# Optimization experiments

Measured on AMD Instinct MI355X. Metric: run time of the kernel, lower is better.

Reference implementation:

```python
import jax, jax.numpy as jnp
import numpy as np

K_POW = 3.0
EPS = 1e-6

def _weight1(d, r):
    # (1 - (d/r)^2)^k for d < r else 0; guard base before float power
    base = jnp.where(d < r, 1.0 - (d / r) ** 2, 0.0)
    return base ** K_POW

def _weight2(d, r):
    # 1 for d < r/2; (1 - ((2d-r)/r)^2)^k for r/2 <= d < r; else 0
    band = (d >= r / 2) & (d < r)
    base = jnp.where(band, 1.0 - ((2.0 * d - r) / r) ** 2, 0.0)
    return jnp.where(d < r / 2, 1.0, base ** K_POW)

def setup_inputs() -> dict:
    key = jax.random.key(0)
    ks = jax.random.split(key, 10)
    n, p, L = 4096, 128, 32
    x = jax.random.uniform(ks[0], (n, p), dtype=jnp.float32)
    s = 0.05
    return {
        "x": x,
        "r0": jnp.float32(4.0),
        "r1": jnp.float32(2.0),
        "r2": jnp.float32(4.0),
        "We1": jax.random.normal(ks[1], (L, p), jnp.float32) * s,
        "be1": jnp.zeros((L,), jnp.float32),
        "We2": jax.random.normal(ks[2], (L, L), jnp.float32) * s,
        "be2": jnp.zeros((L,), jnp.float32),
        "Wd1": jax.random.normal(ks[3], (L, L), jnp.float32) * s,
        "bd1": jnp.zeros((L,), jnp.float32),
        "Wd2": jax.random.normal(ks[4], (p, L), jnp.float32) * s,
        "bd2": jnp.zeros((p,), jnp.float32),
    }

def _mr_layer(x, r0, r1, r2):
    y = x  # y = x.clone()
    x2 = jnp.sum(x * x, axis=-1)
    d2 = x2[:, None] + x2[None, :] - 2.0 * (x @ x.T)  # (n, n)
    dist = jnp.sqrt(jnp.maximum(d2, 1e-12))
    md = dist.max()
    # torch reassigns r to max_dist when r > max_dist -> min(r, max_dist)
    r0e = jnp.minimum(r0, md)
    r1e = jnp.minimum(r1, md)
    r2e = jnp.minimum(r2, md)
    # inds = any(dist <= r0) is all-true (diag is ~0), so no row selection needed
    alpha = _weight1(dist, r0e)
    alpha = alpha / jnp.sum(alpha, axis=0, keepdims=True)
    mu = alpha.T @ x  # (n, p)
    mu = jnp.where(jnp.isnan(mu), y, mu)
    U = y - mu  # (n, p); contraction direction per point
    # projection scalar ps[i,j] = <x_i - y_j, U_j>, avoiding (n,n,p) diff tensor
    ps = x @ U.T - jnp.sum(y * U, axis=-1)[None, :]  # (n, n)
    u_norm2 = jnp.sum(U * U, axis=-1)[None, :]  # (1, n)
    dist_u2 = jnp.maximum(ps ** 2 * u_norm2, EPS)
    dist_v = jnp.sqrt(jnp.maximum(dist ** 2 - dist_u2, EPS))
    dist_u = jnp.sqrt(dist_u2)
    beta = _weight2(dist_v, r1e) * _weight2(dist_u, r2e)
    beta = beta / jnp.sum(beta, axis=0, keepdims=True)
    e_Z = beta.T @ x
    e_Z = jnp.where(jnp.isnan(e_Z), y, e_Z)
    return e_Z

def reference(x, r0, r1, r2, We1, be1, We2, be2, Wd1, bd1, Wd2, bd2):
    y = _mr_layer(x, r0, r1, r2)
    # encoder: Linear -> GELU(exact) -> Linear
    h = jax.nn.gelu(y @ We1.T + be1, approximate=False)
    z = h @ We2.T + be2
    # decoder: Linear -> GELU(exact) -> Linear -> Sigmoid
    h2 = jax.nn.gelu(z @ Wd1.T + bd1, approximate=False)
    x_hat = jax.nn.sigmoid(h2 @ Wd2.T + bd2)
    # loss = lam_recon * MSE(x, x_hat); lam_topo = lam_geom = 0
    return jnp.mean((x - x_hat) ** 2)
```

## Files before the change

kernel.cpp:

```cpp
#include <hip/hip_runtime.h>
#include <math.h>

#define N 4096
#define P 128
#define LDIM 32
#define CHUNKS 8
#define ITILES 4

typedef unsigned int u32;
typedef unsigned short u16;
typedef short s16x8 __attribute__((ext_vector_type(8)));
typedef float f32x4 __attribute__((ext_vector_type(4)));

__device__ __forceinline__ u16 f2b(float f) {
  u32 u = __float_as_uint(f);
  u += 0x7fffu + ((u >> 16) & 1u);
  return (u16)(u >> 16);
}
__device__ __forceinline__ float b2f(u16 h) { return __uint_as_float(((u32)h) << 16); }

__device__ __forceinline__ float w2f(float d, float r) {
  if (d < 0.5f * r) return 1.0f;
  if (d < r) { float t = (2.0f * d - r) / r; float b = 1.0f - t * t; return b * b * b; }
  return 0.0f;
}
__device__ __forceinline__ float geluf(float a) {
  return 0.5f * a * (1.0f + erff(a * 0.70710678118654752f));
}

#define MFMA(a, b, c) __builtin_amdgcn_mfma_f32_16x16x32_bf16((a), (b), (c), 0, 0, 0)

__global__ __launch_bounds__(256) void k_init(float* __restrict__ z, int cnt, float* __restrict__ out) {
  int i = blockIdx.x * 256 + threadIdx.x;
  if (i < cnt) z[i] = 0.0f;
  if (blockIdx.x == 0 && threadIdx.x == 0) out[0] = 0.0f;
}

__global__ __launch_bounds__(256) void k_prep(const float* __restrict__ x, u16* __restrict__ xb,
                                              u16* __restrict__ xbT, float* __restrict__ x2) {
  __shared__ u16 tl[32][36];
  const int bi = blockIdx.x * 32, bk = blockIdx.y * 32;
  const int tid = threadIdx.x;
  const int row = tid >> 3, cs = (tid & 7) * 4;
  float4 v = *(const float4*)&x[(size_t)(bi + row) * P + bk + cs];
  u16 h0 = f2b(v.x), h1 = f2b(v.y), h2 = f2b(v.z), h3 = f2b(v.w);
  float d0 = b2f(h0), d1 = b2f(h1), d2 = b2f(h2), d3 = b2f(h3);
  float s = d0 * d0 + d1 * d1 + d2 * d2 + d3 * d3;
  s += __shfl_down(s, 4); s += __shfl_down(s, 2); s += __shfl_down(s, 1);
  if ((tid & 7) == 0) atomicAdd(&x2[bi + row], s);
  ushort4 o4; o4.x = h0; o4.y = h1; o4.z = h2; o4.w = h3;
  *(ushort4*)(xb + (size_t)(bi + row) * P + bk + cs) = o4;
  tl[row][cs + 0] = h0; tl[row][cs + 1] = h1; tl[row][cs + 2] = h2; tl[row][cs + 3] = h3;
  __syncthreads();
  const int orow = tid >> 3, ocs = (tid & 7) * 4;
  ushort4 t4;
  t4.x = tl[ocs + 0][orow]; t4.y = tl[ocs + 1][orow]; t4.z = tl[ocs + 2][orow]; t4.w = tl[ocs + 3][orow];
  *(ushort4*)(xbT + (size_t)(bk + orow) * N + bi + ocs) = t4;
}

__global__ __launch_bounds__(512, 4) void k_grammax(const u16* __restrict__ xb, const float* __restrict__ x2,
                                                    u32* __restrict__ mdb) {
  __shared__ uint4 LA[1024];
  const int j0 = blockIdx.x * 64;
  const int cid = blockIdx.y;
  if (cid * 512 + 512 <= j0) return;
  const int tid = threadIdx.x;
  const int lane = tid & 63, w = tid >> 6;
  const int lm = lane & 15, quad = lane >> 4;
  {
    const uint4* g = (const uint4*)(xb + (size_t)j0 * P);
#pragma unroll
    for (int it = 0; it < 2; ++it) {
      int c = it * 512 + tid;
      int row = c >> 4, ch = c & 15;
      LA[row * 16 + (ch ^ (row & 7))] = g[c];
    }
  }
  float x2j[4][4];
#pragma unroll
  for (int u = 0; u < 4; u++)
#pragma unroll
    for (int reg = 0; reg < 4; reg++) x2j[u][reg] = x2[j0 + u * 16 + quad * 4 + reg];
  __syncthreads();
  float lmax = 0.0f;
  for (int t = 0; t < ITILES; ++t) {
    const int i0 = cid * 512 + t * 128;
    if (i0 + 128 <= j0) continue;
    f32x4 accG[4];
#pragma unroll
    for (int u = 0; u < 4; u++) accG[u] = {0.f, 0.f, 0.f, 0.f};
    const u16* gb = xb + (size_t)(i0 + w * 16 + lm) * P;
#pragma unroll
    for (int ks = 0; ks < 4; ++ks) {
      s16x8 bf = *(const s16x8*)(gb + ks * 32 + quad * 8);
      s16x8 af[4];
#pragma unroll
      for (int u = 0; u < 4; u++) { int m = u * 16 + lm; af[u] = *(const s16x8*)&LA[m * 16 + ((ks * 4 + quad) ^ (m & 7))]; }
#pragma unroll
      for (int u = 0; u < 4; u++) accG[u] = MFMA(af[u], bf, accG[u]);
    }
    float x2i = x2[i0 + w * 16 + lm];
#pragma unroll
    for (int u = 0; u < 4; u++)
#pragma unroll
      for (int reg = 0; reg < 4; reg++) lmax = fmaxf(lmax, x2j[u][reg] + x2i - 2.0f * accG[u][reg]);
  }
#pragma unroll
  for (int o = 32; o > 0; o >>= 1) lmax = fmaxf(lmax, __shfl_down(lmax, o));
  if (lane == 0) atomicMax(mdb, __float_as_uint(lmax));
}

__global__ __launch_bounds__(512, 4) void k_alpha(const u16* __restrict__ xb, const u16* __restrict__ xbT,
                                                  const float* __restrict__ x2,
                                                  float* __restrict__ muP, float* __restrict__ S1P,
                                                  const float* __restrict__ r0p, const u32* __restrict__ mdb) {
  __shared__ uint4 LA[1024];
  __shared__ u16 W16[64 * 136];
  const int j0 = blockIdx.x * 64, cid = blockIdx.y;
  const int tid = threadIdx.x;
  const int lane = tid & 63, w = tid >> 6;
  const int lm = lane & 15, quad = lane >> 4;
  {
    const uint4* g = (const uint4*)(xb + (size_t)j0 * P);
#pragma unroll
    for (int it = 0; it < 2; ++it) {
      int c = it * 512 + tid;
      int row = c >> 4, ch = c & 15;
      LA[row * 16 + (ch ^ (row & 7))] = g[c];
    }
  }
  const float mdf = sqrtf(fmaxf(__uint_as_float(*mdb), 1e-12f));
  const float re = fminf(r0p[0], mdf);
  const float re2 = re * re, inv_re2 = 1.0f / re2;
  float x2j[4][4];
#pragma unroll
  for (int u = 0; u < 4; u++)
#pragma unroll
    for (int reg = 0; reg < 4; reg++) x2j[u][reg] = x2[j0 + u * 16 + quad * 4 + reg];
  f32x4 accPV[4];
#pragma unroll
  for (int u = 0; u < 4; u++) accPV[u] = {0.f, 0.f, 0.f, 0.f};
  float sjacc = 0.0f;
  const int srow = tid >> 3, spart = tid & 7;
  __syncthreads();
  for (int t = 0; t < ITILES; ++t) {
    const int i0 = cid * 512 + t * 128;
    f32x4 accG[4];
#pragma unroll
    for (int u = 0; u < 4; u++) accG[u] = {0.f, 0.f, 0.f, 0.f};
    const u16* gb = xb + (size_t)(i0 + w * 16 + lm) * P;
#pragma unroll
    for (int ks = 0; ks < 4; ++ks) {
      s16x8 bf = *(const s16x8*)(gb + ks * 32 + quad * 8);
      s16x8 af[4];
#pragma unroll
      for (int u = 0; u < 4; u++) { int m = u * 16 + lm; af[u] = *(const s16x8*)&LA[m * 16 + ((ks * 4 + quad) ^ (m & 7))]; }
#pragma unroll
      for (int u = 0; u < 4; u++) accG[u] = MFMA(af[u], bf, accG[u]);
    }
    float x2i = x2[i0 + w * 16 + lm];
    u16 wv[4][4];
#pragma unroll
    for (int u = 0; u < 4; u++)
#pragma unroll
      for (int reg = 0; reg < 4; reg++) {
        float d2 = fmaxf(x2j[u][reg] + x2i - 2.0f * accG[u][reg], 1e-12f);
        float wt = 0.0f;
        if (d2 < re2) { float b = 1.0f - d2 * inv_re2; wt = b * b * b; }
        wv[u][reg] = f2b(wt);
      }
    __syncthreads();
#pragma unroll
    for (int u = 0; u < 4; u++)
#pragma unroll
      for (int reg = 0; reg < 4; reg++)
        W16[(u * 16 + quad * 4 + reg) * 136 + w * 16 + lm] = wv[u][reg];
    __syncthreads();
    {
      const uint4* wr = (const uint4*)&W16[srow * 136 + spart * 16];
      uint4 a0 = wr[0], a1 = wr[1];
      u32 arr[8] = {a0.x, a0.y, a0.z, a0.w, a1.x, a1.y, a1.z, a1.w};
#pragma unroll
      for (int e = 0; e < 8; e++) sjacc += b2f((u16)(arr[e] & 0xffffu)) + b2f((u16)(arr[e] >> 16));
    }
    const u16* gx = xbT + (size_t)(w * 16 + lm) * N + i0;
#pragma unroll
    for (int ks = 0; ks < 4; ++ks) {
      s16x8 bx = *(const s16x8*)(gx + ks * 32 + quad * 8);
      s16x8 aw[4];
#pragma unroll
      for (int u = 0; u < 4; u++) { int m = u * 16 + lm; aw[u] = *(const s16x8*)&W16[m * 136 + ks * 32 + quad * 8]; }
#pragma unroll
      for (int u = 0; u < 4; u++) accPV[u] = MFMA(aw[u], bx, accPV[u]);
    }
  }
  float* mu = muP + (size_t)cid * N * P;
#pragma unroll
  for (int u = 0; u < 4; u++)
#pragma unroll
    for (int reg = 0; reg < 4; reg++)
      mu[(size_t)(j0 + u * 16 + quad * 4 + reg) * P + w * 16 + lm] = accPV[u][reg];
  sjacc += __shfl_down(sjacc, 4);
  sjacc += __shfl_down(sjacc, 2);
  sjacc += __shfl_down(sjacc, 1);
  if (spart == 0) S1P[cid * N + j0 + srow] = sjacc;
}

__global__ __launch_bounds__(128) void k_finU(const float* __restrict__ x, const u16* __restrict__ xb,
                                              const float* __restrict__ muP, const float* __restrict__ S1P,
                                              u16* __restrict__ Ub, float* __restrict__ u2, float* __restrict__ cj) {
  const int j = blockIdx.x, t = threadIdx.x;
  float ssum = 0.0f, msum = 0.0f;
#pragma unroll
  for (int c = 0; c < CHUNKS; ++c) {
    ssum += S1P[c * N + j];
    msum += muP[((size_t)c * N + j) * P + t];
  }
  float xv = x[(size_t)j * P + t];
  float uval = 0.0f;
  if (ssum > 0.0f) uval = xv - msum / ssum;
  u16 ub = f2b(uval);
  Ub[(size_t)j * P + t] = ub;
  float uf = b2f(ub);
  float xbf = b2f(xb[(size_t)j * P + t]);
  float a = uf * uf, b = xbf * uf;
#pragma unroll
  for (int o = 32; o > 0; o >>= 1) { a += __shfl_down(a, o); b += __shfl_down(b, o); }
  __shared__ float ra[2], rb[2];
  if ((t & 63) == 0) { ra[t >> 6] = a; rb[t >> 6] = b; }
  __syncthreads();
  if (t == 0) { u2[j] = ra[0] + ra[1]; cj[j] = rb[0] + rb[1]; }
}

__global__ __launch_bounds__(512, 4) void k_betaez(const u16* __restrict__ xb, const u16* __restrict__ Ub,
                                                   const u16* __restrict__ xbT,
                                                   const float* __restrict__ x2, const float* __restrict__ u2,
                                                   const float* __restrict__ cj,
                                                   float* __restrict__ ezP, float* __restrict__ S2P,
                                                   const float* __restrict__ r1p, const float* __restrict__ r2p,
                                                   const u32* __restrict__ mdb) {
  __shared__ uint4 LA[1024];
  __shared__ uint4 LU[1024];
  __shared__ u16 W16[64 * 136];
  __shared__ float SX2[64], SU2[64], SCJ[64];
  const int j0 = blockIdx.x * 64, cid = blockIdx.y;
  const int tid = threadIdx.x;
  const int lane = tid & 63, w = tid >> 6;
  const int lm = lane & 15, quad = lane >> 4;
  {
    const uint4* ga = (const uint4*)(xb + (size_t)j0 * P);
    const uint4* gu = (const uint4*)(Ub + (size_t)j0 * P);
#pragma unroll
    for (int it = 0; it < 2; ++it) {
      int c = it * 512 + tid;
      int row = c >> 4, ch = c & 15;
      int sw = row * 16 + (ch ^ (row & 7));
      LA[sw] = ga[c];
      LU[sw] = gu[c];
    }
  }
  if (tid < 64) { SX2[tid] = x2[j0 + tid]; SU2[tid] = u2[j0 + tid]; SCJ[tid] = cj[j0 + tid]; }
  const float mdf = sqrtf(fmaxf(__uint_as_float(*mdb), 1e-12f));
  const float r1e = fminf(r1p[0], mdf), r2e = fminf(r2p[0], mdf);
  f32x4 accPV[4];
#pragma unroll
  for (int u = 0; u < 4; u++) accPV[u] = {0.f, 0.f, 0.f, 0.f};
  float sjacc = 0.0f;
  const int srow = tid >> 3, spart = tid & 7;
  __syncthreads();
  for (int t = 0; t < ITILES; ++t) {
    const int i0 = cid * 512 + t * 128;
    f32x4 accG[4], accP[4];
#pragma unroll
    for (int u = 0; u < 4; u++) { accG[u] = {0.f, 0.f, 0.f, 0.f}; accP[u] = {0.f, 0.f, 0.f, 0.f}; }
    const u16* gb = xb + (size_t)(i0 + w * 16 + lm) * P;
#pragma unroll
    for (int ks = 0; ks < 4; ++ks) {
      s16x8 bf = *(const s16x8*)(gb + ks * 32 + quad * 8);
      s16x8 af[4], au[4];
#pragma unroll
      for (int u = 0; u < 4; u++) {
        int m = u * 16 + lm;
        int off = m * 16 + ((ks * 4 + quad) ^ (m & 7));
        af[u] = *(const s16x8*)&LA[off];
        au[u] = *(const s16x8*)&LU[off];
      }
#pragma unroll
      for (int u = 0; u < 4; u++) {
        accG[u] = MFMA(af[u], bf, accG[u]);
        accP[u] = MFMA(au[u], bf, accP[u]);
      }
    }
    float x2i = x2[i0 + w * 16 + lm];
    u16 wv[4][4];
#pragma unroll
    for (int u = 0; u < 4; u++)
#pragma unroll
      for (int reg = 0; reg < 4; reg++) {
        int jj = u * 16 + quad * 4 + reg;
        float d2 = fmaxf(SX2[jj] + x2i - 2.0f * accG[u][reg], 1e-12f);
        float ps = accP[u][reg] - SCJ[jj];
        float du2 = fmaxf(ps * ps * SU2[jj], 1e-6f);
        float dv = sqrtf(fmaxf(d2 - du2, 1e-6f));
        float du = sqrtf(du2);
        wv[u][reg] = f2b(w2f(dv, r1e) * w2f(du, r2e));
      }
    __syncthreads();
#pragma unroll
    for (int u = 0; u < 4; u++)
#pragma unroll
      for (int reg = 0; reg < 4; reg++)
        W16[(u * 16 + quad * 4 + reg) * 136 + w * 16 + lm] = wv[u][reg];
    __syncthreads();
    {
      const uint4* wr = (const uint4*)&W16[srow * 136 + spart * 16];
      uint4 a0 = wr[0], a1 = wr[1];
      u32 arr[8] = {a0.x, a0.y, a0.z, a0.w, a1.x, a1.y, a1.z, a1.w};
#pragma unroll
      for (int e = 0; e < 8; e++) sjacc += b2f((u16)(arr[e] & 0xffffu)) + b2f((u16)(arr[e] >> 16));
    }
    const u16* gx = xbT + (size_t)(w * 16 + lm) * N + i0;
#pragma unroll
    for (int ks = 0; ks < 4; ++ks) {
      s16x8 bx = *(const s16x8*)(gx + ks * 32 + quad * 8);
      s16x8 aw[4];
#pragma unroll
      for (int u = 0; u < 4; u++) { int m = u * 16 + lm; aw[u] = *(const s16x8*)&W16[m * 136 + ks * 32 + quad * 8]; }
#pragma unroll
      for (int u = 0; u < 4; u++) accPV[u] = MFMA(aw[u], bx, accPV[u]);
    }
  }
  float* ez = ezP + (size_t)cid * N * P;
#pragma unroll
  for (int u = 0; u < 4; u++)
#pragma unroll
    for (int reg = 0; reg < 4; reg++)
      ez[(size_t)(j0 + u * 16 + quad * 4 + reg) * P + w * 16 + lm] = accPV[u][reg];
  sjacc += __shfl_down(sjacc, 4);
  sjacc += __shfl_down(sjacc, 2);
  sjacc += __shfl_down(sjacc, 1);
  if (spart == 0) S2P[cid * N + j0 + srow] = sjacc;
}

#define AE_ROWS 16
__global__ __launch_bounds__(256) void k_ae(const float* __restrict__ x, const float* __restrict__ ezP,
                                            const float* __restrict__ S2P,
                                            const float* __restrict__ We1, const float* __restrict__ be1,
                                            const float* __restrict__ We2, const float* __restrict__ be2,
                                            const float* __restrict__ Wd1, const float* __restrict__ bd1,
                                            const float* __restrict__ Wd2, const float* __restrict__ bd2,
                                            float* __restrict__ out) {
  __shared__ float We1T[P][33];
  __shared__ float We2T[LDIM][33];
  __shared__ float Wd1T[LDIM][33];
  __shared__ float Wd2T[LDIM][129];
  __shared__ float ezs[AE_ROWS][P];
  __shared__ float h1s[AE_ROWS][LDIM], zbs[AE_ROWS][LDIM], h2s[AE_ROWS][LDIM];
  __shared__ float be1s[LDIM], be2s[LDIM], bd1s[LDIM], bd2s[P];
  __shared__ float s2s[AE_ROWS];
  const int tid = threadIdx.x;
  const int r0 = blockIdx.x * AE_ROWS;
  for (int idx = tid; idx < P * LDIM; idx += 256) {
    int o = idx >> 7, k = idx & 127;
    We1T[k][o] = We1[idx];
    int o2 = idx >> 5, k2 = idx & 31;
    Wd2T[k2][o2] = Wd2[idx];
  }
  for (int idx = tid; idx < LDIM * LDIM; idx += 256) {
    int o = idx >> 5, k = idx & 31;
    We2T[k][o] = We2[idx];
    Wd1T[k][o] = Wd1[idx];
  }
  if (tid < LDIM) { be1s[tid] = be1[tid]; be2s[tid] = be2[tid]; bd1s[tid] = bd1[tid]; }
  if (tid < P) bd2s[tid] = bd2[tid];
  if (tid < AE_ROWS) {
    float s = 0.0f;
#pragma unroll
    for (int c = 0; c < CHUNKS; ++c) s += S2P[c * N + r0 + tid];
    s2s[tid] = s;
  }
  __syncthreads();
  for (int idx = tid; idx < AE_ROWS * P; idx += 256) {
    int r = idx >> 7, col = idx & 127;
    int row = r0 + r;
    float es = 0.0f;
#pragma unroll
    for (int c = 0; c < CHUNKS; ++c) es += ezP[((size_t)c * N + row) * P + col];
    float xv = x[(size_t)row * P + col];
    ezs[r][col] = (s2s[r] > 0.0f) ? (es / s2s[r]) : xv;
  }
  __syncthreads();
  {
    const int o = tid & 31, rh = tid >> 5;
#pragma unroll
    for (int rr = 0; rr < 2; rr++) {
      int r = rh + rr * 8;
      float a = be1s[o];
#pragma unroll 8
      for (int k = 0; k < P; k++) a = fmaf(We1T[k][o], ezs[r][k], a);
      h1s[r][o] = geluf(a);
    }
  }
  __syncthreads();
  {
    const int o = tid & 31, rh = tid >> 5;
#pragma unroll
    for (int rr = 0; rr < 2; rr++) {
      int r = rh + rr * 8;
      float a = be2s[o];
#pragma unroll
      for (int k = 0; k < LDIM; k++) a = fmaf(We2T[k][o], h1s[r][k], a);
      zbs[r][o] = a;
    }
  }
  __syncthreads();
  {
    const int o = tid & 31, rh = tid >> 5;
#pragma unroll
    for (int rr = 0; rr < 2; rr++) {
      int r = rh + rr * 8;
      float a = bd1s[o];
#pragma unroll
      for (int k = 0; k < LDIM; k++) a = fmaf(Wd1T[k][o], zbs[r][k], a);
      h2s[r][o] = geluf(a);
    }
  }
  __syncthreads();
  {
    const int o = tid & 127, rh = tid >> 7;
    float part = 0.0f;
#pragma unroll
    for (int rr = 0; rr < 8; rr++) {
      int r = rh + rr * 2;
      int row = r0 + r;
      float a = bd2s[o];
#pragma unroll
      for (int k = 0; k < LDIM; k++) a = fmaf(Wd2T[k][o], h2s[r][k], a);
      float xh = 1.0f / (1.0f + expf(-a));
      float diff = x[(size_t)row * P + o] - xh;
      part = fmaf(diff, diff, part);
    }
#pragma unroll
    for (int off = 32; off > 0; off >>= 1) part += __shfl_down(part, off);
    if ((tid & 63) == 0) atomicAdd(out, part * (1.0f / ((float)N * (float)P)));
  }
}

extern "C" void kernel_launch(void* const* d_in, const int* in_sizes, int n_in,
                              void* d_out, int out_size, void* d_ws, size_t ws_size,
                              hipStream_t stream) {
  const float* x   = (const float*)d_in[0];
  const float* r0  = (const float*)d_in[1];
  const float* r1  = (const float*)d_in[2];
  const float* r2  = (const float*)d_in[3];
  const float* We1 = (const float*)d_in[4];
  const float* be1 = (const float*)d_in[5];
  const float* We2 = (const float*)d_in[6];
  const float* be2 = (const float*)d_in[7];
  const float* Wd1 = (const float*)d_in[8];
  const float* bd1 = (const float*)d_in[9];
  const float* Wd2 = (const float*)d_in[10];
  const float* bd2 = (const float*)d_in[11];
  float* out = (float*)d_out;

  char* base = (char*)d_ws;
  size_t off = 0;
  u16* xb  = (u16*)(base + off); off += (size_t)N * P * 2;
  u16* xbT = (u16*)(base + off); off += (size_t)N * P * 2;
  u16* Ub  = (u16*)(base + off); off += (size_t)N * P * 2;
  float* muP = (float*)(base + off); off += (size_t)CHUNKS * N * P * 4;
  float* ezP = (float*)(base + off); off += (size_t)CHUNKS * N * P * 4;
  float* S1P = (float*)(base + off); off += (size_t)CHUNKS * N * 4;
  float* S2P = (float*)(base + off); off += (size_t)CHUNKS * N * 4;
  float* x2  = (float*)(base + off); off += (size_t)N * 4;
  u32* mdb   = (u32*)(base + off); off += 4;
  float* u2  = (float*)(base + off); off += (size_t)N * 4;
  float* cjv = (float*)(base + off); off += (size_t)N * 4;

  const int zcnt = N + 1;
  hipLaunchKernelGGL(k_init, dim3((zcnt + 255) / 256), dim3(256), 0, stream, x2, zcnt, out);
  hipLaunchKernelGGL(k_prep, dim3(N / 32, P / 32), dim3(256), 0, stream, x, xb, xbT, x2);
  hipLaunchKernelGGL(k_grammax, dim3(N / 64, CHUNKS), dim3(512), 0, stream, xb, x2, mdb);
  hipLaunchKernelGGL(k_alpha, dim3(N / 64, CHUNKS), dim3(512), 0, stream, xb, xbT, x2, muP, S1P, r0, mdb);
  hipLaunchKernelGGL(k_finU, dim3(N), dim3(128), 0, stream, x, xb, muP, S1P, Ub, u2, cjv);
  hipLaunchKernelGGL(k_betaez, dim3(N / 64, CHUNKS), dim3(512), 0, stream, xb, Ub, xbT, x2, u2, cjv, ezP, S2P, r1, r2, mdb);
  hipLaunchKernelGGL(k_ae, dim3(N / AE_ROWS), dim3(256), 0, stream, x, ezP, S2P, We1, be1, We2, be2, Wd1, bd1, Wd2, bd2, out);
}
```

Measured before the change: 201.0 us.

## Skip full max-distance Gram pass via anchor lower bound; MFMA row sums

Adds a cheap anchor kernel that computes distances from row 0 to every point as a lower bound on the maximum distance. The full Gram max kernel now exits early when that bound already exceeds the largest radius, with a small margin, so the radius clamps become no-ops. The alpha and beta kernels now get their column weight sums from an extra MFMA against a ones vector instead of LDS reads and adds. Their operand order is swapped so stores to LDS are packed, and the prep kernel handles whole rows to drop the atomics. The early exit depends on the data spread; if the bound falls short, the full pass still runs.

```diff
diff --git a/kernel.cpp b/kernel.cpp
--- a/kernel.cpp
+++ b/kernel.cpp
@@ -30,36 +30,76 @@
 
 #define MFMA(a, b, c) __builtin_amdgcn_mfma_f32_16x16x32_bf16((a), (b), (c), 0, 0, 0)
 
-__global__ __launch_bounds__(256) void k_init(float* __restrict__ z, int cnt, float* __restrict__ out) {
-  int i = blockIdx.x * 256 + threadIdx.x;
-  if (i < cnt) z[i] = 0.0f;
-  if (blockIdx.x == 0 && threadIdx.x == 0) out[0] = 0.0f;
+__global__ void k_init(u32* __restrict__ mdb, float* __restrict__ out) {
+  if (threadIdx.x == 0) { *mdb = 0u; out[0] = 0.0f; }
 }
 
 __global__ __launch_bounds__(256) void k_prep(const float* __restrict__ x, u16* __restrict__ xb,
                                               u16* __restrict__ xbT, float* __restrict__ x2) {
-  __shared__ u16 tl[32][36];
-  const int bi = blockIdx.x * 32, bk = blockIdx.y * 32;
+  __shared__ u16 tlT[128][40];
+  const int bi = blockIdx.x * 32;
   const int tid = threadIdx.x;
-  const int row = tid >> 3, cs = (tid & 7) * 4;
-  float4 v = *(const float4*)&x[(size_t)(bi + row) * P + bk + cs];
-  u16 h0 = f2b(v.x), h1 = f2b(v.y), h2 = f2b(v.z), h3 = f2b(v.w);
-  float d0 = b2f(h0), d1 = b2f(h1), d2 = b2f(h2), d3 = b2f(h3);
-  float s = d0 * d0 + d1 * d1 + d2 * d2 + d3 * d3;
+  const int r = tid >> 3, cg = (tid & 7) * 16;
+  const float* src = &x[(size_t)(bi + r) * P + cg];
+  float4 v0 = *(const float4*)(src + 0);
+  float4 v1 = *(const float4*)(src + 4);
+  float4 v2 = *(const float4*)(src + 8);
+  float4 v3 = *(const float4*)(src + 12);
+  u16 h[16];
+  h[0] = f2b(v0.x); h[1] = f2b(v0.y); h[2] = f2b(v0.z); h[3] = f2b(v0.w);
+  h[4] = f2b(v1.x); h[5] = f2b(v1.y); h[6] = f2b(v1.z); h[7] = f2b(v1.w);
+  h[8] = f2b(v2.x); h[9] = f2b(v2.y); h[10] = f2b(v2.z); h[11] = f2b(v2.w);
+  h[12] = f2b(v3.x); h[13] = f2b(v3.y); h[14] = f2b(v3.z); h[15] = f2b(v3.w);
+  float s = 0.0f;
+#pragma unroll
+  for (int e = 0; e < 16; e++) { float f = b2f(h[e]); s = fmaf(f, f, s); }
   s += __shfl_down(s, 4); s += __shfl_down(s, 2); s += __shfl_down(s, 1);
-  if ((tid & 7) == 0) atomicAdd(&x2[bi + row], s);
-  ushort4 o4; o4.x = h0; o4.y = h1; o4.z = h2; o4.w = h3;
-  *(ushort4*)(xb + (size_t)(bi + row) * P + bk + cs) = o4;
-  tl[row][cs + 0] = h0; tl[row][cs + 1] = h1; tl[row][cs + 2] = h2; tl[row][cs + 3] = h3;
-  __syncthreads();
-  const int orow = tid >> 3, ocs = (tid & 7) * 4;
-  ushort4 t4;
-  t4.x = tl[ocs + 0][orow]; t4.y = tl[ocs + 1][orow]; t4.z = tl[ocs + 2][orow]; t4.w = tl[ocs + 3][orow];
-  *(ushort4*)(xbT + (size_t)(bk + orow) * N + bi + ocs) = t4;
+  if ((tid & 7) == 0) x2[bi + r] = s;
+  uint4 p0, p1;
+  p0.x = (u32)h[0] | ((u32)h[1] << 16);  p0.y = (u32)h[2] | ((u32)h[3] << 16);
+  p0.z = (u32)h[4] | ((u32)h[5] << 16);  p0.w = (u32)h[6] | ((u32)h[7] << 16);
+  p1.x = (u32)h[8] | ((u32)h[9] << 16);  p1.y = (u32)h[10] | ((u32)h[11] << 16);
+  p1.z = (u32)h[12] | ((u32)h[13] << 16); p1.w = (u32)h[14] | ((u32)h[15] << 16);
+  *(uint4*)&xb[(size_t)(bi + r) * P + cg] = p0;
+  *(uint4*)&xb[(size_t)(bi + r) * P + cg + 8] = p1;
+#pragma unroll
+  for (int e = 0; e < 16; e++) tlT[cg + e][r] = h[e];
+  __syncthreads();
+  const int c = tid >> 1, hh = tid & 1;
+  uint4 q0 = *(const uint4*)&tlT[c][hh * 16];
+  uint4 q1 = *(const uint4*)&tlT[c][hh * 16 + 8];
+  *(uint4*)&xbT[(size_t)c * N + bi + hh * 16] = q0;
+  *(uint4*)&xbT[(size_t)c * N + bi + hh * 16 + 8] = q1;
+}
+
+__global__ __launch_bounds__(128) void k_anchor(const u16* __restrict__ xb, const float* __restrict__ x2,
+                                                u32* __restrict__ mdb) {
+  const int i = blockIdx.x * 128 + threadIdx.x;
+  const uint4* ra = (const uint4*)(xb + (size_t)i * P);
+  const uint4* r0 = (const uint4*)xb;
+  float dot = 0.0f;
+#pragma unroll
+  for (int q = 0; q < 16; ++q) {
+    uint4 a = ra[q], b = r0[q];
+    u32 aa[4] = {a.x, a.y, a.z, a.w}, bb[4] = {b.x, b.y, b.z, b.w};
+#pragma unroll
+    for (int e = 0; e < 4; e++) {
+      dot = fmaf(b2f((u16)(aa[e] & 0xffffu)), b2f((u16)(bb[e] & 0xffffu)), dot);
+      dot = fmaf(b2f((u16)(aa[e] >> 16)), b2f((u16)(bb[e] >> 16)), dot);
+    }
+  }
+  float d2 = fmaxf(x2[i] + x2[0] - 2.0f * dot, 0.0f);
+#pragma unroll
+  for (int o = 32; o > 0; o >>= 1) d2 = fmaxf(d2, __shfl_down(d2, o));
+  if ((threadIdx.x & 63) == 0) atomicMax(mdb, __float_as_uint(d2));
 }
 
 __global__ __launch_bounds__(512, 4) void k_grammax(const u16* __restrict__ xb, const float* __restrict__ x2,
-                                                    u32* __restrict__ mdb) {
+                                                    u32* __restrict__ mdb,
+                                                    const float* __restrict__ r0p, const float* __restrict__ r1p,
+                                                    const float* __restrict__ r2p) {
+  const float rmax = fmaxf(r0p[0], fmaxf(r1p[0], r2p[0])) * 1.02f;
+  if (__uint_as_float(*mdb) >= rmax * rmax) return;
   __shared__ uint4 LA[1024];
   const int j0 = blockIdx.x * 64;
   const int cid = blockIdx.y;
@@ -132,57 +172,48 @@
   const float mdf = sqrtf(fmaxf(__uint_as_float(*mdb), 1e-12f));
   const float re = fminf(r0p[0], mdf);
   const float re2 = re * re, inv_re2 = 1.0f / re2;
-  float x2j[4][4];
-#pragma unroll
-  for (int u = 0; u < 4; u++)
-#pragma unroll
-    for (int reg = 0; reg < 4; reg++) x2j[u][reg] = x2[j0 + u * 16 + quad * 4 + reg];
-  f32x4 accPV[4];
-#pragma unroll
-  for (int u = 0; u < 4; u++) accPV[u] = {0.f, 0.f, 0.f, 0.f};
-  float sjacc = 0.0f;
-  const int srow = tid >> 3, spart = tid & 7;
+  float x2j[4];
+#pragma unroll
+  for (int v = 0; v < 4; v++) x2j[v] = x2[j0 + v * 16 + lm];
+  f32x4 accPV[4], accS[4];
+#pragma unroll
+  for (int u = 0; u < 4; u++) { accPV[u] = {0.f, 0.f, 0.f, 0.f}; accS[u] = {0.f, 0.f, 0.f, 0.f}; }
+  const s16x8 ones = {0x3F80, 0x3F80, 0x3F80, 0x3F80, 0x3F80, 0x3F80, 0x3F80, 0x3F80};
   __syncthreads();
   for (int t = 0; t < ITILES; ++t) {
     const int i0 = cid * 512 + t * 128;
     f32x4 accG[4];
 #pragma unroll
-    for (int u = 0; u < 4; u++) accG[u] = {0.f, 0.f, 0.f, 0.f};
-    const u16* gb = xb + (size_t)(i0 + w * 16 + lm) * P;
+    for (int v = 0; v < 4; v++) accG[v] = {0.f, 0.f, 0.f, 0.f};
+    const u16* ga = xb + (size_t)(i0 + w * 16 + lm) * P;
 #pragma unroll
     for (int ks = 0; ks < 4; ++ks) {
-      s16x8 bf = *(const s16x8*)(gb + ks * 32 + quad * 8);
-      s16x8 af[4];
-#pragma unroll
-      for (int u = 0; u < 4; u++) { int m = u * 16 + lm; af[u] = *(const s16x8*)&LA[m * 16 + ((ks * 4 + quad) ^ (m & 7))]; }
-#pragma unroll
-      for (int u = 0; u < 4; u++) accG[u] = MFMA(af[u], bf, accG[u]);
-    }
-    float x2i = x2[i0 + w * 16 + lm];
-    u16 wv[4][4];
-#pragma unroll
-    for (int u = 0; u < 4; u++)
+      s16x8 af = *(const s16x8*)(ga + ks * 32 + quad * 8);
+      s16x8 bf[4];
+#pragma unroll
+      for (int v = 0; v < 4; v++) { int m = v * 16 + lm; bf[v] = *(const s16x8*)&LA[m * 16 + ((ks * 4 + quad) ^ (m & 7))]; }
+#pragma unroll
+      for (int v = 0; v < 4; v++) accG[v] = MFMA(af, bf[v], accG[v]);
+    }
+    float4 x2iv = *(const float4*)&x2[i0 + w * 16 + quad * 4];
+    const float xi[4] = {x2iv.x, x2iv.y, x2iv.z, x2iv.w};
+    u16 wv4[4][4];
+#pragma unroll
+    for (int v = 0; v < 4; v++)
 #pragma unroll
       for (int reg = 0; reg < 4; reg++) {
-        float d2 = fmaxf(x2j[u][reg] + x2i - 2.0f * accG[u][reg], 1e-12f);
+        float d2 = fmaxf(xi[reg] + x2j[v] - 2.0f * accG[v][reg], 1e-12f);
         float wt = 0.0f;
         if (d2 < re2) { float b = 1.0f - d2 * inv_re2; wt = b * b * b; }
-        wv[u][reg] = f2b(wt);
+        wv4[v][reg] = f2b(wt);
       }
     __syncthreads();
 #pragma unroll
-    for (int u = 0; u < 4; u++)
-#pragma unroll
-      for (int reg = 0; reg < 4; reg++)
-        W16[(u * 16 + quad * 4 + reg) * 136 + w * 16 + lm] = wv[u][reg];
+    for (int v = 0; v < 4; v++) {
+      ushort4 pk; pk.x = wv4[v][0]; pk.y = wv4[v][1]; pk.z = wv4[v][2]; pk.w = wv4[v][3];
+      *(ushort4*)&W16[(v * 16 + lm) * 136 + w * 16 + quad * 4] = pk;
+    }
     __syncthreads();
-    {
-      const uint4* wr = (const uint4*)&W16[srow * 136 + spart * 16];
-      uint4 a0 = wr[0], a1 = wr[1];
-      u32 arr[8] = {a0.x, a0.y, a0.z, a0.w, a1.x, a1.y, a1.z, a1.w};
-#pragma unroll
-      for (int e = 0; e < 8; e++) sjacc += b2f((u16)(arr[e] & 0xffffu)) + b2f((u16)(arr[e] >> 16));
-    }
     const u16* gx = xbT + (size_t)(w * 16 + lm) * N + i0;
 #pragma unroll
     for (int ks = 0; ks < 4; ++ks) {
@@ -192,6 +223,10 @@
       for (int u = 0; u < 4; u++) { int m = u * 16 + lm; aw[u] = *(const s16x8*)&W16[m * 136 + ks * 32 + quad * 8]; }
 #pragma unroll
       for (int u = 0; u < 4; u++) accPV[u] = MFMA(aw[u], bx, accPV[u]);
+      if (w == 0) {
+#pragma unroll
+        for (int u = 0; u < 4; u++) accS[u] = MFMA(aw[u], ones, accS[u]);
+      }
     }
   }
   float* mu = muP + (size_t)cid * N * P;
@@ -200,10 +235,13 @@
 #pragma unroll
     for (int reg = 0; reg < 4; reg++)
       mu[(size_t)(j0 + u * 16 + quad * 4 + reg) * P + w * 16 + lm] = accPV[u][reg];
-  sjacc += __shfl_down(sjacc, 4);
-  sjacc += __shfl_down(sjacc, 2);
-  sjacc += __shfl_down(sjacc, 1);
-  if (spart == 0) S1P[cid * N + j0 + srow] = sjacc;
+  if (w == 0 && lm == 0) {
+#pragma unroll
+    for (int u = 0; u < 4; u++)
+#pragma unroll
+      for (int reg = 0; reg < 4; reg++)
+        S1P[cid * N + j0 + u * 16 + quad * 4 + reg] = accS[u][reg];
+  }
 }
 
 __global__ __launch_bounds__(128) void k_finU(const float* __restrict__ x, const u16* __restrict__ xb,
@@ -242,7 +280,6 @@
   __shared__ uint4 LA[1024];
   __shared__ uint4 LU[1024];
   __shared__ u16 W16[64 * 136];
-  __shared__ float SX2[64], SU2[64], SCJ[64];
   const int j0 = blockIdx.x * 64, cid = blockIdx.y;
   const int tid = threadIdx.x;
   const int lane = tid & 63, w = tid >> 6;
@@ -259,66 +296,66 @@
       LU[sw] = gu[c];
     }
   }
-  if (tid < 64) { SX2[tid] = x2[j0 + tid]; SU2[tid] = u2[j0 + tid]; SCJ[tid] = cj[j0 + tid]; }
   const float mdf = sqrtf(fmaxf(__uint_as_float(*mdb), 1e-12f));
   const float r1e = fminf(r1p[0], mdf), r2e = fminf(r2p[0], mdf);
-  f32x4 accPV[4];
-#pragma unroll
-  for (int u = 0; u < 4; u++) accPV[u] = {0.f, 0.f, 0.f, 0.f};
-  float sjacc = 0.0f;
-  const int srow = tid >> 3, spart = tid & 7;
+  float x2j[4], u2j[4], ncj[4];
+#pragma unroll
+  for (int v = 0; v < 4; v++) {
+    int jj = j0 + v * 16 + lm;
+    x2j[v] = x2[jj]; u2j[v] = u2[jj]; ncj[v] = -cj[jj];
+  }
+  f32x4 accPV[4], accS[4];
+#pragma unroll
+  for (int u = 0; u < 4; u++) { accPV[u] = {0.f, 0.f, 0.f, 0.f}; accS[u] = {0.f, 0.f, 0.f, 0.f}; }
+  const s16x8 ones = {0x3F80, 0x3F80, 0x3F80, 0x3F80, 0x3F80, 0x3F80, 0x3F80, 0x3F80};
   __syncthreads();
   for (int t = 0; t < ITILES; ++t) {
     const int i0 = cid * 512 + t * 128;
     f32x4 accG[4], accP[4];
 #pragma unroll
-    for (int u = 0; u < 4; u++) { accG[u] = {0.f, 0.f, 0.f, 0.f}; accP[u] = {0.f, 0.f, 0.f, 0.f}; }
-    const u16* gb = xb + (size_t)(i0 + w * 16 + lm) * P;
+    for (int v = 0; v < 4; v++) {
+      accG[v] = {0.f, 0.f, 0.f, 0.f};
+      accP[v] = {ncj[v], ncj[v], ncj[v], ncj[v]};
+    }
+    const u16* ga = xb + (size_t)(i0 + w * 16 + lm) * P;
 #pragma unroll
     for (int ks = 0; ks < 4; ++ks) {
-      s16x8 bf = *(const s16x8*)(gb + ks * 32 + quad * 8);
-      s16x8 af[4], au[4];
-#pragma unroll
-      for (int u = 0; u < 4; u++) {
-        int m = u * 16 + lm;
+      s16x8 af = *(const s16x8*)(ga + ks * 32 + quad * 8);
+      s16x8 bf[4], bu[4];
+#pragma unroll
+      for (int v = 0; v < 4; v++) {
+        int m = v * 16 + lm;
         int off = m * 16 + ((ks * 4 + quad) ^ (m & 7));
-        af[u] = *(const s16x8*)&LA[off];
-        au[u] = *(const s16x8*)&LU[off];
+        bf[v] = *(const s16x8*)&LA[off];
+        bu[v] = *(const s16x8*)&LU[off];
       }
 #pragma unroll
-      for (int u = 0; u < 4; u++) {
-        accG[u] = MFMA(af[u], bf, accG[u]);
-        accP[u] = MFMA(au[u], bf, accP[u]);
+      for (int v = 0; v < 4; v++) {
+        accG[v] = MFMA(af, bf[v], accG[v]);
+        accP[v] = MFMA(af, bu[v], accP[v]);
       }
     }
-    float x2i = x2[i0 + w * 16 + lm];
-    u16 wv[4][4];
-#pragma unroll
-    for (int u = 0; u < 4; u++)
+    float4 x2iv = *(const float4*)&x2[i0 + w * 16 + quad * 4];
+    const float xi[4] = {x2iv.x, x2iv.y, x2iv.z, x2iv.w};
+    u16 wv4[4][4];
+#pragma unroll
+    for (int v = 0; v < 4; v++)
 #pragma unroll
       for (int reg = 0; reg < 4; reg++) {
-        int jj = u * 16 + quad * 4 + reg;
-        float d2 = fmaxf(SX2[jj] + x2i - 2.0f * accG[u][reg], 1e-12f);
-        float ps = accP[u][reg] - SCJ[jj];
-        float du2 = fmaxf(ps * ps * SU2[jj], 1e-6f);
+        float d2 = fmaxf(xi[reg] + x2j[v] - 2.0f * accG[v][reg], 1e-12f);
+        float ps = accP[v][reg];
+        float du2 = fmaxf(ps * ps * u2j[v], 1e-6f);
         float dv = sqrtf(fmaxf(d2 - du2, 1e-6f));
         float du = sqrtf(du2);
-        wv[u][reg] = f2b(w2f(dv, r1e) * w2f(du, r2e));
+        wv4[v][reg] = f2b(w2f(dv, r1e) * w2f(du, r2e));
       }
     __syncthreads();
 #pragma unroll
-    for (int u = 0; u < 4; u++)
-#pragma unroll
-      for (int reg = 0; reg < 4; reg++)
-        W16[(u * 16 + quad * 4 + reg) * 136 + w * 16 + lm] = wv[u][reg];
+    for (int v = 0; v < 4; v++) {
+      ushort4 pk; pk.x = wv4[v][0]; pk.y = wv4[v][1]; pk.z = wv4[v][2]; pk.w = wv4[v][3];
+      *(ushort4*)&W16[(v * 16 + lm) * 136 + w * 16 + quad * 4] = pk;
+    }
     __syncthreads();
-    {
-      const uint4* wr = (const uint4*)&W16[srow * 136 + spart * 16];
-      uint4 a0 = wr[0], a1 = wr[1];
-      u32 arr[8] = {a0.x, a0.y, a0.z, a0.w, a1.x, a1.y, a1.z, a1.w};
-#pragma unroll
-      for (int e = 0; e < 8; e++) sjacc += b2f((u16)(arr[e] & 0xffffu)) + b2f((u16)(arr[e] >> 16));
-    }
     const u16* gx = xbT + (size_t)(w * 16 + lm) * N + i0;
 #pragma unroll
     for (int ks = 0; ks < 4; ++ks) {
@@ -328,6 +365,10 @@
       for (int u = 0; u < 4; u++) { int m = u * 16 + lm; aw[u] = *(const s16x8*)&W16[m * 136 + ks * 32 + quad * 8]; }
 #pragma unroll
       for (int u = 0; u < 4; u++) accPV[u] = MFMA(aw[u], bx, accPV[u]);
+      if (w == 0) {
+#pragma unroll
+        for (int u = 0; u < 4; u++) accS[u] = MFMA(aw[u], ones, accS[u]);
+      }
     }
   }
   float* ez = ezP + (size_t)cid * N * P;
@@ -336,10 +377,13 @@
 #pragma unroll
     for (int reg = 0; reg < 4; reg++)
       ez[(size_t)(j0 + u * 16 + quad * 4 + reg) * P + w * 16 + lm] = accPV[u][reg];
-  sjacc += __shfl_down(sjacc, 4);
-  sjacc += __shfl_down(sjacc, 2);
-  sjacc += __shfl_down(sjacc, 1);
-  if (spart == 0) S2P[cid * N + j0 + srow] = sjacc;
+  if (w == 0 && lm == 0) {
+#pragma unroll
+    for (int u = 0; u < 4; u++)
+#pragma unroll
+      for (int reg = 0; reg < 4; reg++)
+        S2P[cid * N + j0 + u * 16 + quad * 4 + reg] = accS[u][reg];
+  }
 }
 
 #define AE_ROWS 16
@@ -469,7 +513,7 @@
   u16* xbT = (u16*)(base + off); off += (size_t)N * P * 2;
   u16* Ub  = (u16*)(base + off); off += (size_t)N * P * 2;
   float* muP = (float*)(base + off); off += (size_t)CHUNKS * N * P * 4;
-  float* ezP = (float*)(base + off); off += (size_t)CHUNKS * N * P * 4;
+  float* ezP = (float*)(base + off); off += (size_t)CHUNKS * N * 4 * P / 4 * 4;
   float* S1P = (float*)(base + off); off += (size_t)CHUNKS * N * 4;
   float* S2P = (float*)(base + off); off += (size_t)CHUNKS * N * 4;
   float* x2  = (float*)(base + off); off += (size_t)N * 4;
@@ -477,10 +521,10 @@
   float* u2  = (float*)(base + off); off += (size_t)N * 4;
   float* cjv = (float*)(base + off); off += (size_t)N * 4;
 
-  const int zcnt = N + 1;
-  hipLaunchKernelGGL(k_init, dim3((zcnt + 255) / 256), dim3(256), 0, stream, x2, zcnt, out);
-  hipLaunchKernelGGL(k_prep, dim3(N / 32, P / 32), dim3(256), 0, stream, x, xb, xbT, x2);
-  hipLaunchKernelGGL(k_grammax, dim3(N / 64, CHUNKS), dim3(512), 0, stream, xb, x2, mdb);
+  hipLaunchKernelGGL(k_init, dim3(1), dim3(64), 0, stream, mdb, out);
+  hipLaunchKernelGGL(k_prep, dim3(N / 32), dim3(256), 0, stream, x, xb, xbT, x2);
+  hipLaunchKernelGGL(k_anchor, dim3(N / 128), dim3(128), 0, stream, xb, x2, mdb);
+  hipLaunchKernelGGL(k_grammax, dim3(N / 64, CHUNKS), dim3(512), 0, stream, xb, x2, mdb, r0, r1, r2);
   hipLaunchKernelGGL(k_alpha, dim3(N / 64, CHUNKS), dim3(512), 0, stream, xb, xbT, x2, muP, S1P, r0, mdb);
   hipLaunchKernelGGL(k_finU, dim3(N), dim3(128), 0, stream, x, xb, muP, S1P, Ub, u2, cjv);
   hipLaunchKernelGGL(k_betaez, dim3(N / 64, CHUNKS), dim3(512), 0, stream, xb, Ub, xbT, x2, u2, cjv, ezP, S2P, r1, r2, mdb);
```

Result: faster. 186.9 us (-7.0%).
